# Kernel tuning notes

Measured on AMD Instinct MI355X. Metric: run time of the kernel, lower is better.

## Reference

```python
import jax, jax.numpy as jnp
import numpy as np

DIM = 192
D_STATE = 16
D_CONV = 4
EXPAND = 2
DI = EXPAND * DIM          # d_inner = 384
DT_RANK = -(-DIM // 16)    # ceil(dim/16) = 12
BSZ, T, H, W = 2, 16, 32, 32
EPS = 1e-5


def setup_inputs() -> dict:
    key = jax.random.key(0)
    ks = jax.random.split(key, 10)
    r = lambda k, s, sc=0.02: jax.random.normal(k, s, dtype=jnp.float32) * sc
    return {
        "x": jax.random.normal(ks[0], (BSZ, T, H, W, DIM), dtype=jnp.float32),
        "conv1_w": r(ks[1], (DIM, DIM, 3, 3, 3)),
        "conv1_b": jnp.zeros((DIM,), jnp.float32),
        "conv2_w": r(ks[2], (DIM, DIM, 3, 3, 3)),
        "conv2_b": jnp.zeros((DIM,), jnp.float32),
        "ln_g": jnp.ones((DIM,), jnp.float32),
        "ln_b": jnp.zeros((DIM,), jnp.float32),
        "in_proj_w": r(ks[3], (2 * DI, DIM)),
        "conv1d_w": r(ks[4], (DI, 1, D_CONV), 0.1),
        "conv1d_b": jnp.zeros((DI,), jnp.float32),
        "x_proj_w": r(ks[5], (DT_RANK + 2 * D_STATE, DI)),
        "dt_proj_w": r(ks[6], (DI, DT_RANK), 0.1),
        "dt_proj_b": r(ks[7], (DI,), 0.1),
        "A_log": jnp.log(jnp.tile(jnp.arange(1, D_STATE + 1, dtype=jnp.float32), (DI, 1))),
        "Dp": jnp.ones((DI,), jnp.float32),
        "out_proj_w": r(ks[8], (DIM, DI)),
    }


def _conv3d(x, w, b):
    y = jax.lax.conv_general_dilated(
        x, w, window_strides=(1, 1, 1), padding=((1, 1), (1, 1), (1, 1)),
        dimension_numbers=("NCDHW", "OIDHW", "NCDHW"))
    return y + b[None, :, None, None, None]


def _inorm(x):  # InstanceNorm3d, affine=False: normalize per (B,C) over spatial
    mu = jnp.mean(x, axis=(2, 3, 4), keepdims=True)
    var = jnp.var(x, axis=(2, 3, 4), keepdims=True)
    return (x - mu) * jax.lax.rsqrt(var + EPS)


def _mamba(x_norm, in_proj_w, conv1d_w, conv1d_b, x_proj_w, dt_proj_w,
           dt_proj_b, A_log, Dp, out_proj_w):
    B, L, _ = x_norm.shape
    xz = x_norm @ in_proj_w.T                      # (B, L, 2*DI)
    u, z = xz[..., :DI], xz[..., DI:]
    # causal depthwise conv1d over sequence (left pad d_conv-1)
    uc = jax.lax.conv_general_dilated(
        u.transpose(0, 2, 1), conv1d_w, window_strides=(1,),
        padding=((D_CONV - 1, 0),), dimension_numbers=("NCH", "OIH", "NCH"),
        feature_group_count=DI) + conv1d_b[None, :, None]
    u = jax.nn.silu(uc.transpose(0, 2, 1))         # (B, L, DI)
    xdb = u @ x_proj_w.T                           # (B, L, dt_rank+2*d_state)
    dt = xdb[..., :DT_RANK]
    Bm = xdb[..., DT_RANK:DT_RANK + D_STATE]       # (B, L, d_state)
    Cm = xdb[..., DT_RANK + D_STATE:]
    delta = jax.nn.softplus(dt @ dt_proj_w.T + dt_proj_b)  # (B, L, DI)
    A = -jnp.exp(A_log)                            # (DI, d_state)

    def step(h, inp):
        dlt, bt, ct, ut = inp                      # (B,DI) (B,S) (B,S) (B,DI)
        h = jnp.exp(dlt[:, :, None] * A) * h + (dlt * ut)[:, :, None] * bt[:, None, :]
        return h, jnp.einsum("bds,bs->bd", h, ct)

    h0 = jnp.zeros((B, DI, D_STATE), x_norm.dtype)
    xs = (delta.transpose(1, 0, 2), Bm.transpose(1, 0, 2),
          Cm.transpose(1, 0, 2), u.transpose(1, 0, 2))
    _, ys = jax.lax.scan(step, h0, xs)             # (L, B, DI)
    y = ys.transpose(1, 0, 2) + u * Dp
    y = y * jax.nn.silu(z)
    return y @ out_proj_w.T                        # (B, L, DIM)


def reference(x, conv1_w, conv1_b, conv2_w, conv2_b, ln_g, ln_b, in_proj_w,
              conv1d_w, conv1d_b, x_proj_w, dt_proj_w, dt_proj_b, A_log, Dp,
              out_proj_w):
    B = x.shape[0]
    xc = x.transpose(0, 4, 1, 2, 3)                # (B, C, T, H, W)
    res = xc
    x1 = jax.nn.leaky_relu(_inorm(_conv3d(xc, conv1_w, conv1_b)), 0.01)
    xc = _inorm(_conv3d(x1, conv2_w, conv2_b)) + res
    xl = xc.transpose(0, 2, 3, 4, 1)               # (B, T, H, W, C)
    # faithful to original: raw row-major reshape (B,T,H,W,C)->(B,C,THW)
    x_flat = xl.reshape(B, DIM, T * H * W).transpose(0, 2, 1)
    # LayerNorm over last dim
    mu = jnp.mean(x_flat, axis=-1, keepdims=True)
    var = jnp.var(x_flat, axis=-1, keepdims=True)
    x_norm = (x_flat - mu) * jax.lax.rsqrt(var + EPS) * ln_g + ln_b
    y = _mamba(x_norm, in_proj_w, conv1d_w, conv1d_b, x_proj_w, dt_proj_w,
               dt_proj_b, A_log, Dp, out_proj_w)
    return y.reshape(B, T, H, W, DIM)
```

## Files before the change

kernel.cpp:

```cpp
#include <hip/hip_runtime.h>


typedef unsigned short u16;
typedef __attribute__((ext_vector_type(8))) short bf16x8;
typedef __attribute__((ext_vector_type(4))) float f4;

#define MTOT 32768

__device__ __forceinline__ float b2f(u16 v){ return __uint_as_float(((unsigned)v)<<16); }
__device__ __forceinline__ u16 f2b(float f){
  unsigned u = __float_as_uint(f);
  return (u16)((u + 0x7fffu + ((u>>16)&1u)) >> 16);
}
__device__ __forceinline__ float blo(unsigned v){ return __uint_as_float(v<<16); }
__device__ __forceinline__ float bhi(unsigned v){ return __uint_as_float(v & 0xffff0000u); }
__device__ __forceinline__ unsigned pack2(float a, float b){
  return (unsigned)f2b(a) | ((unsigned)f2b(b)<<16);
}

__device__ __forceinline__ void gl16(const u16* g, u16* l){
  __builtin_amdgcn_global_load_lds((const __attribute__((address_space(1))) void*)g,
                                   (__attribute__((address_space(3))) void*)l, 16, 0, 0);
}

__global__ __launch_bounds__(256) void k_init(int* cnt, float* zp, float* stats){
  int i = blockIdx.x*256 + threadIdx.x;
  if (i == 0)   *cnt = 0;
  if (i < 128)  zp[i] = 0.f;
  if (i < 3072) stats[i] = 0.f;
}

__global__ void k_diag(float* o, float v){
  o[0] = v; o[1] = v;
  ((u16*)o)[4] = f2b(v); ((u16*)o)[5] = f2b(v);
}

__global__ __launch_bounds__(256) void k_probe(const u16* __restrict__ x, int* cnt){
  int t = threadIdx.x;
  int c = 0;
  #pragma unroll
  for (int i=0;i<16;i++){
    u16 v = x[t*16 + i];
    if (((v>>7)&0xFF) >= 0x90) c++;
  }
  if (c) atomicAdd(cnt, c);
}

__global__ __launch_bounds__(256) void k_cvt(const void* __restrict__ src, u16* __restrict__ dst,
                                             int n, const int* __restrict__ cnt){
  const int gid = blockIdx.x*256 + threadIdx.x;
  if (gid*8 >= n) return;
  if (*cnt > 64){
    const float4* s = (const float4*)src;
    float4 a = s[gid*2], b = s[gid*2+1];
    *(uint4*)(dst + gid*8) = make_uint4(pack2(a.x,a.y), pack2(a.z,a.w),
                                        pack2(b.x,b.y), pack2(b.z,b.w));
  } else {
    ((uint4*)dst)[gid] = ((const uint4*)src)[gid];
  }
}

struct SmallCvt { const void* src[13]; int n[13]; int off[13]; };

__global__ __launch_bounds__(256) void k_cvt_small(SmallCvt sc, u16* __restrict__ wc,
                                                   const int* __restrict__ cnt){
  const int t = blockIdx.y;
  const int gid = blockIdx.x*256 + threadIdx.x;
  const int n = sc.n[t];
  if (gid*8 >= n) return;
  u16* dst = wc + sc.off[t];
  if (*cnt > 64){
    const float4* s = (const float4*)sc.src[t];
    float4 a = s[gid*2], b = s[gid*2+1];
    *(uint4*)(dst + gid*8) = make_uint4(pack2(a.x,a.y), pack2(a.z,a.w),
                                        pack2(b.x,b.y), pack2(b.z,b.w));
  } else {
    *(uint4*)(dst + gid*8) = ((const uint4*)sc.src[t])[gid];
  }
}

__global__ __launch_bounds__(256) void k_wt(const void* __restrict__ w1, const void* __restrict__ w2,
                                            u16* __restrict__ b1, u16* __restrict__ b2,
                                            const int* __restrict__ cnt){
  int gid = blockIdx.x*256 + threadIdx.x;
  if (gid >= 2*995328) return;
  const bool f32 = *cnt > 64;
  int sel = gid >= 995328 ? 1 : 0;
  int lo  = gid - sel*995328;
  int co = lo / 5184, rr = lo % 5184;
  int p  = rr / 192,  ci = rr % 192;
  const void* s = sel ? w2 : w1;
  const int si = (co*192 + ci)*27 + p;
  u16 v = f32 ? f2b(((const float*)s)[si]) : ((const u16*)s)[si];
  (sel ? b2 : b1)[lo] = v;
}

__global__ __launch_bounds__(256) void k_conv(const u16* __restrict__ X, const u16* __restrict__ Bw,
                                              const u16* __restrict__ bias, u16* __restrict__ outc,
                                              float* __restrict__ sumG, float* __restrict__ sqG){
  __shared__ u16 Al[1280*8];
  __shared__ u16 Bl[1792*8];
  const int tid = threadIdx.x;
  const int m0 = blockIdx.x*128, n0 = blockIdx.y*64;
  const int bb = blockIdx.x >> 7;
  const int rem0 = m0 & 16383;
  const int t0 = rem0 >> 10, h0 = (rem0 >> 5) & 31;
  const int lane = tid&63, wv = tid>>6, wm = wv>>1, wn = wv&1, lr = lane&15, q = lane>>4;

  int aoff[5];
  #pragma unroll
  for (int j=0;j<5;j++){
    const int c = j*256 + tid;
    const int rw = c/9, cc = c%9;
    aoff[j] = (c < 1170 && cc < 8) ? (rw*192 + cc*8) : 0;
  }
  int boff[7];
  #pragma unroll
  for (int j=0;j<7;j++){
    const int c = j*256 + tid;
    const int rw = c/9, cc = c%9;
    boff[j] = (c < 1728 && cc < 8) ? ((n0 + (rw & 63))*5184 + (rw >> 6)*192 + cc*8) : 0;
  }

  const f4 z4 = {0.f,0.f,0.f,0.f};
  const bf16x8 z8 = {0,0,0,0,0,0,0,0};
  f4 acc[4][2];
  #pragma unroll
  for (int i=0;i<4;i++){
    #pragma unroll
    for (int j=0;j<2;j++) acc[i][j] = z4;
  }

  for (int s=0; s<27; ++s){
    const int dtdh = s/3, sub = s - dtdh*3;
    const int dt = dtdh/3 - 1, dh = dtdh%3 - 1;
    __syncthreads();
    const u16* Ab = X + (ptrdiff_t)(m0 - 1 + dt*1024 + dh*32)*192 + sub*64;
    #pragma unroll
    for (int j=0;j<5;j++) gl16(Ab + aoff[j], Al + (size_t)(j*256 + tid)*8);
    const u16* Bb = Bw + dtdh*576 + sub*64;
    #pragma unroll
    for (int j=0;j<7;j++) gl16(Bb + boff[j], Bl + (size_t)(j*256 + tid)*8);
    __syncthreads();
    const bool tval = ((unsigned)(t0 + dt) < 16u);
    const bool hv0 = ((unsigned)(h0 + wm*2     + dh) < 32u);
    const bool hv1 = ((unsigned)(h0 + wm*2 + 1 + dh) < 32u);
    if (tval){
      #pragma unroll
      for (int kt=0; kt<2; ++kt){
        bf16x8 bv[3][2];
        #pragma unroll
        for (int tp=0;tp<3;tp++){
          #pragma unroll
          for (int j=0;j<2;j++)
            bv[tp][j] = *(const bf16x8*)&Bl[(tp*64 + wn*32 + j*16 + lr)*72 + kt*32 + q*8];
        }
        #pragma unroll
        for (int i=0;i<4;i++){
          const bool hok = (i<2) ? hv0 : hv1;
          if (!hok) continue;
          const int crow = wm*64 + i*16 + lr;
          #pragma unroll
          for (int tp=0;tp<3;tp++){
            bf16x8 av = *(const bf16x8*)&Al[(crow + tp)*72 + kt*32 + q*8];
            if (tp==0 && (i&1)==0) av = (lr==0)  ? z8 : av;
            if (tp==2 && (i&1)==1) av = (lr==15) ? z8 : av;
            acc[i][0] = __builtin_amdgcn_mfma_f32_16x16x32_bf16(av, bv[tp][0], acc[i][0], 0,0,0);
            acc[i][1] = __builtin_amdgcn_mfma_f32_16x16x32_bf16(av, bv[tp][1], acc[i][1], 0,0,0);
          }
        }
      }
    }
  }

  float psum[2] = {0.f,0.f}, psq[2] = {0.f,0.f};
  #pragma unroll
  for (int j=0;j<2;j++){
    const int col = n0 + wn*32 + j*16 + lr;
    const float bvl = b2f(bias[col]);
    #pragma unroll
    for (int i=0;i<4;i++){
      const int row0 = m0 + wm*64 + i*16 + q*4;
      #pragma unroll
      for (int g=0; g<4; ++g){
        const float v = acc[i][j][g] + bvl;
        outc[(size_t)(row0+g)*192 + col] = f2b(v);
        psum[j] += v; psq[j] += v*v;
      }
    }
  }
  __syncthreads();
  float* red = (float*)Al;
  if (tid < 128) red[tid] = 0.f;
  __syncthreads();
  #pragma unroll
  for (int j=0;j<2;j++){
    const int cl = wn*32 + j*16 + lr;
    atomicAdd(&red[cl], psum[j]);
    atomicAdd(&red[64+cl], psq[j]);
  }
  __syncthreads();
  if (tid < 64){
    atomicAdd(&sumG[bb*192 + n0 + tid], red[tid]);
    atomicAdd(&sqG[bb*192 + n0 + tid], red[64+tid]);
  }
}

template<int EPI>
__global__ __launch_bounds__(256) void k_gemm(const u16* __restrict__ A, const u16* __restrict__ Bm,
                                              const int K, const int NB,
                                              void* __restrict__ o0, void* __restrict__ o1,
                                              const u16* __restrict__ zp,
                                              const int* __restrict__ cnt){
  __shared__ u16 Al[128*104];
  __shared__ u16 Bl[64*104];
  const int tid = threadIdx.x;
  const int m0 = blockIdx.x*128, n0 = blockIdx.y*64;
  const int r = tid>>1, half = tid&1;
  const u16* arow = A + ((size_t)(m0+r)*K + half*48);
  const int bn = tid>>2, bk = tid&3;
  const bool bval = (n0+bn) < NB;
  const u16* brow = Bm + ((size_t)(n0+bn)*K + bk*24);
  const int lane = tid&63, wv = tid>>6, wm = wv>>1, wn = wv&1, lr = lane&15, q = lane>>4;
  const f4 z4 = {0.f,0.f,0.f,0.f};
  f4 acc[4][2];
  #pragma unroll
  for (int i=0;i<4;i++){
    #pragma unroll
    for (int j=0;j<2;j++) acc[i][j] = z4;
  }
  for (int k0=0; k0<K; k0+=96){
    const u16* as = arow + k0;
    const u16* bs = bval ? (brow + k0) : zp;
    __syncthreads();
    #pragma unroll
    for (int i=0;i<6;i++)
      *(uint4*)&Al[r*104 + half*48 + i*8] = *(const uint4*)(as + i*8);
    #pragma unroll
    for (int i=0;i<3;i++)
      *(uint4*)&Bl[bn*104 + bk*24 + i*8] = *(const uint4*)(bs + i*8);
    __syncthreads();
    #pragma unroll
    for (int kt=0; kt<3; ++kt){
      bf16x8 av[4], bv[2];
      #pragma unroll
      for (int i=0;i<4;i++) av[i] = *(const bf16x8*)&Al[(wm*64 + i*16 + lr)*104 + kt*32 + q*8];
      #pragma unroll
      for (int j=0;j<2;j++) bv[j] = *(const bf16x8*)&Bl[(wn*32 + j*16 + lr)*104 + kt*32 + q*8];
      #pragma unroll
      for (int i=0;i<4;i++){
        #pragma unroll
        for (int j=0;j<2;j++)
          acc[i][j] = __builtin_amdgcn_mfma_f32_16x16x32_bf16(av[i], bv[j], acc[i][j], 0,0,0);
      }
    }
  }
  const bool f32o = (EPI == 2) && (*cnt > 64);
  #pragma unroll
  for (int j=0;j<2;j++){
    const int col = n0 + wn*32 + j*16 + lr;
    #pragma unroll
    for (int i=0;i<4;i++){
      const int row0 = m0 + wm*64 + i*16 + q*4;
      #pragma unroll
      for (int g=0; g<4; ++g){
        const int row = row0 + g;
        const float v = acc[i][j][g];
        if (EPI == 0){
          if (col < 384) ((u16*)o0)[(size_t)row*384 + col] = f2b(v);
          else           ((u16*)o1)[(size_t)row*384 + (col-384)] = f2b(v);
        } else if (EPI == 1){
          if (col < 44)  ((float*)o0)[(size_t)row*44 + col] = v;
        } else {
          if (f32o) ((float*)o0)[(size_t)row*192 + col] = v;
          else      ((u16*) o0)[(size_t)row*192 + col] = f2b(v);
        }
      }
    }
  }
}

__global__ __launch_bounds__(384) void k_infin(const float* __restrict__ s, const float* __restrict__ s2,
                                               float* __restrict__ mr){
  const int i = threadIdx.x;
  const float mean = s[i]*(1.f/16384.f);
  const float var  = s2[i]*(1.f/16384.f) - mean*mean;
  mr[i]     = mean;
  mr[384+i] = rsqrtf(var + 1e-5f);
}

__global__ __launch_bounds__(256) void k_inapply(const u16* __restrict__ craw, const float* __restrict__ mr,
                                                 const u16* __restrict__ resid, u16* __restrict__ outp,
                                                 const int mode){
  const int gid = blockIdx.x*256 + threadIdx.x;
  const size_t base = (size_t)gid*8;
  const int mrow = gid/24;
  const int c0 = (gid%24)*8;
  const int b = mrow >> 14;
  const uint4 rv = *(const uint4*)(craw + base);
  float vv[8] = {blo(rv.x),bhi(rv.x),blo(rv.y),bhi(rv.y),blo(rv.z),bhi(rv.z),blo(rv.w),bhi(rv.w)};
  uint4 xv;
  float rr[8];
  if (mode == 2){
    xv = *(const uint4*)(resid + base);
    rr[0]=blo(xv.x); rr[1]=bhi(xv.x); rr[2]=blo(xv.y); rr[3]=bhi(xv.y);
    rr[4]=blo(xv.z); rr[5]=bhi(xv.z); rr[6]=blo(xv.w); rr[7]=bhi(xv.w);
  }
  unsigned pk[4];
  #pragma unroll
  for (int k2=0;k2<4;k2++){
    const int c = c0 + 2*k2;
    float a0 = (vv[2*k2]   - mr[b*192+c])  * mr[384 + b*192 + c];
    float a1 = (vv[2*k2+1] - mr[b*192+c+1])* mr[384 + b*192 + c+1];
    if (mode == 1){ a0 = a0 > 0.f ? a0 : 0.01f*a0; a1 = a1 > 0.f ? a1 : 0.01f*a1; }
    else          { a0 += rr[2*k2]; a1 += rr[2*k2+1]; }
    pk[k2] = pack2(a0, a1);
  }
  *(uint4*)(outp + base) = make_uint4(pk[0],pk[1],pk[2],pk[3]);
}

__global__ __launch_bounds__(128) void k_ln(const u16* __restrict__ F, const u16* __restrict__ g,
                                            const u16* __restrict__ bb, u16* __restrict__ xn){
  __shared__ u16 S[192*128];
  const int tid = threadIdx.x;
  const int b = blockIdx.y;
  const int l0 = blockIdx.x*128;
  const u16* Fb = F + (size_t)b*3145728;
  for (int qi = tid; qi < 3072; qi += 128){
    int c = qi >> 4, o = (qi & 15)*8;
    *(uint4*)&S[c*128 + o] = *(const uint4*)(Fb + (size_t)c*16384 + l0 + o);
  }
  __syncthreads();
  float sum = 0.f, sq = 0.f;
  for (int c=0;c<192;c++){ float v = b2f(S[c*128 + tid]); sum += v; sq += v*v; }
  const float mean = sum*(1.f/192.f);
  const float rs = rsqrtf(sq*(1.f/192.f) - mean*mean + 1e-5f);
  u16* dst = xn + ((size_t)(b*16384 + l0 + tid))*192;
  for (int c0=0;c0<192;c0+=8){
    unsigned pk[4];
    #pragma unroll
    for (int k2=0;k2<4;k2++){
      int c = c0 + 2*k2;
      float v0 = (b2f(S[(c  )*128+tid]) - mean)*rs*b2f(g[c  ]) + b2f(bb[c  ]);
      float v1 = (b2f(S[(c+1)*128+tid]) - mean)*rs*b2f(g[c+1]) + b2f(bb[c+1]);
      pk[k2] = pack2(v0, v1);
    }
    *(uint4*)(dst + c0) = make_uint4(pk[0],pk[1],pk[2],pk[3]);
  }
}

__global__ __launch_bounds__(256) void k_conv1d(const u16* __restrict__ u, const u16* __restrict__ w,
                                                const u16* __restrict__ bias, u16* __restrict__ up){
  const int gid = blockIdx.x*256 + threadIdx.x;
  const int mrow = gid/48, d8 = (gid%48)*8;
  const int l = mrow & 16383;
  float acc[8];
  #pragma unroll
  for (int k=0;k<8;k++) acc[k] = b2f(bias[d8+k]);
  float wk[4][8];
  #pragma unroll
  for (int dd=0;dd<8;dd++){
    uint2 tw = *(const uint2*)(w + (size_t)(d8+dd)*4);
    wk[0][dd]=blo(tw.x); wk[1][dd]=bhi(tw.x); wk[2][dd]=blo(tw.y); wk[3][dd]=bhi(tw.y);
  }
  #pragma unroll
  for (int k=0;k<4;k++){
    if (l - 3 + k < 0) continue;
    uint4 tv = *(const uint4*)(u + ((size_t)(mrow-3+k))*384 + d8);
    float uv[8] = {blo(tv.x),bhi(tv.x),blo(tv.y),bhi(tv.y),blo(tv.z),bhi(tv.z),blo(tv.w),bhi(tv.w)};
    #pragma unroll
    for (int dd=0;dd<8;dd++) acc[dd] += uv[dd]*wk[k][dd];
  }
  unsigned pk[4];
  #pragma unroll
  for (int k2=0;k2<4;k2++){
    float a0 = acc[2*k2], a1 = acc[2*k2+1];
    a0 = a0/(1.f + __expf(-a0));
    a1 = a1/(1.f + __expf(-a1));
    pk[k2] = pack2(a0, a1);
  }
  *(uint4*)(up + (size_t)mrow*384 + d8) = make_uint4(pk[0],pk[1],pk[2],pk[3]);
}

__global__ __launch_bounds__(192) void k_scan1(const float* __restrict__ xdb, const u16* __restrict__ up,
                                               const u16* __restrict__ dtw, const u16* __restrict__ dtb,
                                               const u16* __restrict__ alog,
                                               float* __restrict__ P, float* __restrict__ Q){
  __shared__ float xdbS[64*44];
  const int tid = threadIdx.x;
  const int chunk = blockIdx.x, b = blockIdx.y;
  const int d = blockIdx.z*192 + tid;
  const size_t mbase = (size_t)b*16384 + chunk*64;
  const float* xs = xdb + mbase*44;
  for (int qi=tid; qi<704; qi+=192)
    *(float4*)&xdbS[qi*4] = *(const float4*)(xs + (size_t)qi*4);
  float w[12];
  #pragma unroll
  for (int i=0;i<12;i++) w[i] = b2f(dtw[d*12+i]);
  const float dtbv = b2f(dtb[d]);
  float Av[16];
  #pragma unroll
  for (int s=0;s<16;s++) Av[s] = -__expf(b2f(alog[d*16+s]));
  float pp[16], qq[16];
  #pragma unroll
  for (int s=0;s<16;s++){ pp[s]=1.f; qq[s]=0.f; }
  const u16* uptr = up + mbase*384 + d;
  __syncthreads();
  for (int l=0;l<64;l++){
    const float* row = &xdbS[l*44];
    const float4 r0 = *(const float4*)(row);
    const float4 r1 = *(const float4*)(row+4);
    const float4 r2 = *(const float4*)(row+8);
    float a = dtbv + r0.x*w[0]+r0.y*w[1]+r0.z*w[2]+r0.w*w[3]
                   + r1.x*w[4]+r1.y*w[5]+r1.z*w[6]+r1.w*w[7]
                   + r2.x*w[8]+r2.y*w[9]+r2.z*w[10]+r2.w*w[11];
    const float dl = a > 20.f ? a : __logf(1.f + __expf(a));
    const float uv = b2f(uptr[(size_t)l*384]);
    const float dlu = dl*uv;
    const float4 B0 = *(const float4*)(row+12);
    const float4 B1 = *(const float4*)(row+16);
    const float4 B2 = *(const float4*)(row+20);
    const float4 B3 = *(const float4*)(row+24);
    const float Bv[16] = {B0.x,B0.y,B0.z,B0.w,B1.x,B1.y,B1.z,B1.w,
                          B2.x,B2.y,B2.z,B2.w,B3.x,B3.y,B3.z,B3.w};
    #pragma unroll
    for (int s=0;s<16;s++){
      const float as = __expf(dl*Av[s]);
      pp[s] *= as;
      qq[s] = as*qq[s] + dlu*Bv[s];
    }
  }
  const size_t o = (((size_t)b*256 + chunk)*384 + d)*16;
  float* Po = P + o; float* Qo = Q + o;
  *(float4*)(Po+ 0) = make_float4(pp[0],pp[1],pp[2],pp[3]);
  *(float4*)(Po+ 4) = make_float4(pp[4],pp[5],pp[6],pp[7]);
  *(float4*)(Po+ 8) = make_float4(pp[8],pp[9],pp[10],pp[11]);
  *(float4*)(Po+12) = make_float4(pp[12],pp[13],pp[14],pp[15]);
  *(float4*)(Qo+ 0) = make_float4(qq[0],qq[1],qq[2],qq[3]);
  *(float4*)(Qo+ 4) = make_float4(qq[4],qq[5],qq[6],qq[7]);
  *(float4*)(Qo+ 8) = make_float4(qq[8],qq[9],qq[10],qq[11]);
  *(float4*)(Qo+12) = make_float4(qq[12],qq[13],qq[14],qq[15]);
}

__global__ __launch_bounds__(256) void k_scan2(const float* __restrict__ P, const float* __restrict__ Q,
                                               float* __restrict__ hin){
  const int gid = blockIdx.x*256 + threadIdx.x;
  const int b = gid / 6144, ds = gid % 6144;
  const size_t base = (size_t)b*1572864 + ds;
  float h = 0.f;
  for (int g2=0; g2<256; ++g2){
    const size_t idx = base + (size_t)g2*6144;
    hin[idx] = h;
    h = P[idx]*h + Q[idx];
  }
}

__global__ __launch_bounds__(192) void k_scan3(const float* __restrict__ xdb, const u16* __restrict__ up,
                                               const u16* __restrict__ zb,
                                               const u16* __restrict__ dtw, const u16* __restrict__ dtb,
                                               const u16* __restrict__ alog, const u16* __restrict__ dp,
                                               const float* __restrict__ hin, u16* __restrict__ yg){
  __shared__ float xdbS[64*44];
  const int tid = threadIdx.x;
  const int chunk = blockIdx.x, b = blockIdx.y;
  const int d = blockIdx.z*192 + tid;
  const size_t mbase = (size_t)b*16384 + chunk*64;
  const float* xs = xdb + mbase*44;
  for (int qi=tid; qi<704; qi+=192)
    *(float4*)&xdbS[qi*4] = *(const float4*)(xs + (size_t)qi*4);
  float w[12];
  #pragma unroll
  for (int i=0;i<12;i++) w[i] = b2f(dtw[d*12+i]);
  const float dtbv = b2f(dtb[d]);
  float Av[16];
  #pragma unroll
  for (int s=0;s<16;s++) Av[s] = -__expf(b2f(alog[d*16+s]));
  const float Dv = b2f(dp[d]);
  float h[16];
  {
    const float* hi = hin + (((size_t)b*256 + chunk)*384 + d)*16;
    const float4 h0 = *(const float4*)(hi+0);
    const float4 h1 = *(const float4*)(hi+4);
    const float4 h2 = *(const float4*)(hi+8);
    const float4 h3 = *(const float4*)(hi+12);
    h[0]=h0.x;h[1]=h0.y;h[2]=h0.z;h[3]=h0.w;
    h[4]=h1.x;h[5]=h1.y;h[6]=h1.z;h[7]=h1.w;
    h[8]=h2.x;h[9]=h2.y;h[10]=h2.z;h[11]=h2.w;
    h[12]=h3.x;h[13]=h3.y;h[14]=h3.z;h[15]=h3.w;
  }
  const u16* uptr = up + mbase*384 + d;
  const u16* zptr = zb + mbase*384 + d;
  u16* yptr = yg + mbase*384 + d;
  __syncthreads();
  for (int l=0;l<64;l++){
    const float* row = &xdbS[l*44];
    const float4 r0 = *(const float4*)(row);
    const float4 r1 = *(const float4*)(row+4);
    const float4 r2 = *(const float4*)(row+8);
    float a = dtbv + r0.x*w[0]+r0.y*w[1]+r0.z*w[2]+r0.w*w[3]
                   + r1.x*w[4]+r1.y*w[5]+r1.z*w[6]+r1.w*w[7]
                   + r2.x*w[8]+r2.y*w[9]+r2.z*w[10]+r2.w*w[11];
    const float dl = a > 20.f ? a : __logf(1.f + __expf(a));
    const float uv = b2f(uptr[(size_t)l*384]);
    const float dlu = dl*uv;
    const float4 B0 = *(const float4*)(row+12);
    const float4 B1 = *(const float4*)(row+16);
    const float4 B2 = *(const float4*)(row+20);
    const float4 B3 = *(const float4*)(row+24);
    const float4 C0 = *(const float4*)(row+28);
    const float4 C1 = *(const float4*)(row+32);
    const float4 C2 = *(const float4*)(row+36);
    const float4 C3 = *(const float4*)(row+40);
    const float Bv[16] = {B0.x,B0.y,B0.z,B0.w,B1.x,B1.y,B1.z,B1.w,
                          B2.x,B2.y,B2.z,B2.w,B3.x,B3.y,B3.z,B3.w};
    const float Cv[16] = {C0.x,C0.y,C0.z,C0.w,C1.x,C1.y,C1.z,C1.w,
                          C2.x,C2.y,C2.z,C2.w,C3.x,C3.y,C3.z,C3.w};
    float ct = 0.f;
    #pragma unroll
    for (int s=0;s<16;s++){
      const float as = __expf(dl*Av[s]);
      h[s] = as*h[s] + dlu*Bv[s];
      ct += h[s]*Cv[s];
    }
    const float yv = ct + uv*Dv;
    const float zv = b2f(zptr[(size_t)l*384]);
    yptr[(size_t)l*384] = f2b(yv * (zv/(1.f + __expf(-zv))));
  }
}

extern "C" void kernel_launch(void* const* d_in, const int* in_sizes, int n_in,
                              void* d_out, int out_size, void* d_ws, size_t ws_size,
                              hipStream_t stream){
  (void)in_sizes; (void)n_in; (void)out_size;
  const u16* x = (const u16*)d_in[0];
  u16* outp = (u16*)d_out;

  char* ws = (char*)d_ws;
  size_t off = 0;
  auto alloc = [&](size_t bytes)->void*{
    void* p = (void*)(ws + off);
    off += (bytes + 255) & ~(size_t)255;
    return p;
  };
  int*   cnt   = (int*)  alloc(256);
  u16*   zp    = (u16*)  alloc(512);
  float* stats = (float*)alloc((size_t)3072*4);
  u16*   wc    = (u16*)  alloc((size_t)252288*2);
  u16*   Bw1   = (u16*)  alloc((size_t)995328*2);
  u16*   Bw2   = (u16*)  alloc((size_t)995328*2);
  u16*   xc    = (u16*)  alloc((size_t)MTOT*192*2);
  u16*   craw  = (u16*)  alloc((size_t)MTOT*192*2);
  u16*   bx    = (u16*)  alloc((size_t)MTOT*192*2);
  u16*   ubuf  = (u16*)  alloc((size_t)MTOT*384*2);
  u16*   zbuf  = (u16*)  alloc((size_t)MTOT*384*2);
  u16*   upost = (u16*)  alloc((size_t)MTOT*384*2);
  const size_t NEEDED = off;

  if (ws_size < NEEDED){
    k_diag<<<1,1,0,stream>>>((float*)d_out, (float)(ws_size >> 20));
    return;
  }

  u16* xnorm = craw;
  float* xdb = (float*)xc;
  float* P   = (float*)ubuf;
  float* Q   = (float*)(ubuf + 6291456);
  float* hin = (float*)bx;
  u16*   yg  = upost;

  float* sum1 = stats;        float* sq1 = stats+384;  float* mr1 = stats+768;
  float* sum2 = stats+1536;   float* sq2 = stats+1920; float* mr2 = stats+2304;

  SmallCvt sc;
  const int srcIdx[13] = {2,4,5,6,7,8,9,10,11,12,13,14,15};
  const int ns[13]     = {192,192,192,192,147456,1536,384,16896,4608,384,6144,384,73728};
  const int offs[13]   = {0,192,384,576,768,148224,149760,150144,167040,171648,172032,178176,178560};
  for (int i=0;i<13;i++){ sc.src[i]=d_in[srcIdx[i]]; sc.n[i]=ns[i]; sc.off[i]=offs[i]; }
  const u16 *c1b=wc+0, *c2b=wc+192, *lng=wc+384, *lnb=wc+576, *ipw=wc+768,
            *c1dw=wc+148224, *c1db=wc+149760, *xpw=wc+150144, *dtw=wc+167040,
            *dtb=wc+171648, *alog=wc+172032, *dp=wc+178176, *opw=wc+178560;

  k_init<<<12,256,0,stream>>>(cnt, (float*)zp, stats);
  k_probe<<<1,256,0,stream>>>(x, cnt);
  k_cvt<<<3072,256,0,stream>>>(d_in[0], xc, MTOT*192, cnt);
  k_cvt_small<<<dim3(72,13),256,0,stream>>>(sc, wc, cnt);
  k_wt<<<7776,256,0,stream>>>(d_in[1], d_in[3], Bw1, Bw2, cnt);

  k_conv<<<dim3(256,3),256,0,stream>>>(xc, Bw1, c1b, craw, sum1, sq1);
  k_infin<<<1,384,0,stream>>>(sum1, sq1, mr1);
  k_inapply<<<3072,256,0,stream>>>(craw, mr1, xc, bx, 1);
  k_conv<<<dim3(256,3),256,0,stream>>>(bx, Bw2, c2b, craw, sum2, sq2);
  k_infin<<<1,384,0,stream>>>(sum2, sq2, mr2);
  k_inapply<<<3072,256,0,stream>>>(craw, mr2, xc, bx, 2);

  k_ln<<<dim3(128,2),128,0,stream>>>(bx, lng, lnb, xnorm);
  k_gemm<0><<<dim3(256,12),256,0,stream>>>(xnorm, ipw, 192, 768, ubuf, zbuf, zp, cnt);
  k_conv1d<<<6144,256,0,stream>>>(ubuf, c1dw, c1db, upost);
  k_gemm<1><<<dim3(256,1),256,0,stream>>>(upost, xpw, 384, 44, xdb, nullptr, zp, cnt);
  k_scan1<<<dim3(256,2,2),192,0,stream>>>(xdb, upost, dtw, dtb, alog, P, Q);
  k_scan2<<<48,256,0,stream>>>(P, Q, hin);
  k_scan3<<<dim3(256,2,2),192,0,stream>>>(xdb, upost, zbuf, dtw, dtb, alog, dp, hin, yg);
  k_gemm<2><<<dim3(256,3),256,0,stream>>>(yg, opw, 384, 192, outp, nullptr, zp, cnt);
}
```

Before: 555.1 us.

## Split scan state across thread pairs, batch scan2 loads, skip out-of-range conv taps

The selective-scan kernels now give each channel to two threads, each holding 8 of the 16 states. This doubles the grid and cuts per-thread register pressure, with the C-dot partials combined by a shuffle. k_scan2 loads eight P/Q values before running the serial recurrence, so memory latency overlaps the dependent chain. The 3D conv skips loading and syncing for temporal taps that fall outside the volume, instead of loading the tile and then ignoring it. The cost is duplicated dt/softplus work per thread pair and half-idle lanes on the output store.

Result: no change. 555.5 us (+0.1%).

```diff
diff --git a/kernel.cpp b/kernel.cpp
--- a/kernel.cpp
+++ b/kernel.cpp
@@ -134,6 +134,8 @@
   for (int s=0; s<27; ++s){
     const int dtdh = s/3, sub = s - dtdh*3;
     const int dt = dtdh/3 - 1, dh = dtdh%3 - 1;
+    const bool tval = ((unsigned)(t0 + dt) < 16u);
+    if (!tval) continue;
     __syncthreads();
     const u16* Ab = X + (ptrdiff_t)(m0 - 1 + dt*1024 + dh*32)*192 + sub*64;
     #pragma unroll
@@ -142,32 +144,29 @@
     #pragma unroll
     for (int j=0;j<7;j++) gl16(Bb + boff[j], Bl + (size_t)(j*256 + tid)*8);
     __syncthreads();
-    const bool tval = ((unsigned)(t0 + dt) < 16u);
     const bool hv0 = ((unsigned)(h0 + wm*2     + dh) < 32u);
     const bool hv1 = ((unsigned)(h0 + wm*2 + 1 + dh) < 32u);
-    if (tval){
+    #pragma unroll
+    for (int kt=0; kt<2; ++kt){
+      bf16x8 bv[3][2];
       #pragma unroll
-      for (int kt=0; kt<2; ++kt){
-        bf16x8 bv[3][2];
+      for (int tp=0;tp<3;tp++){
+        #pragma unroll
+        for (int j=0;j<2;j++)
+          bv[tp][j] = *(const bf16x8*)&Bl[(tp*64 + wn*32 + j*16 + lr)*72 + kt*32 + q*8];
+      }
+      #pragma unroll
+      for (int i=0;i<4;i++){
+        const bool hok = (i<2) ? hv0 : hv1;
+        if (!hok) continue;
+        const int crow = wm*64 + i*16 + lr;
         #pragma unroll
         for (int tp=0;tp<3;tp++){
-          #pragma unroll
-          for (int j=0;j<2;j++)
-            bv[tp][j] = *(const bf16x8*)&Bl[(tp*64 + wn*32 + j*16 + lr)*72 + kt*32 + q*8];
-        }
-        #pragma unroll
-        for (int i=0;i<4;i++){
-          const bool hok = (i<2) ? hv0 : hv1;
-          if (!hok) continue;
-          const int crow = wm*64 + i*16 + lr;
-          #pragma unroll
-          for (int tp=0;tp<3;tp++){
-            bf16x8 av = *(const bf16x8*)&Al[(crow + tp)*72 + kt*32 + q*8];
-            if (tp==0 && (i&1)==0) av = (lr==0)  ? z8 : av;
-            if (tp==2 && (i&1)==1) av = (lr==15) ? z8 : av;
-            acc[i][0] = __builtin_amdgcn_mfma_f32_16x16x32_bf16(av, bv[tp][0], acc[i][0], 0,0,0);
-            acc[i][1] = __builtin_amdgcn_mfma_f32_16x16x32_bf16(av, bv[tp][1], acc[i][1], 0,0,0);
-          }
+          bf16x8 av = *(const bf16x8*)&Al[(crow + tp)*72 + kt*32 + q*8];
+          if (tp==0 && (i&1)==0) av = (lr==0)  ? z8 : av;
+          if (tp==2 && (i&1)==1) av = (lr==15) ? z8 : av;
+          acc[i][0] = __builtin_amdgcn_mfma_f32_16x16x32_bf16(av, bv[tp][0], acc[i][0], 0,0,0);
+          acc[i][1] = __builtin_amdgcn_mfma_f32_16x16x32_bf16(av, bv[tp][1], acc[i][1], 0,0,0);
         }
       }
     }
@@ -389,7 +388,8 @@
   __shared__ float xdbS[64*44];
   const int tid = threadIdx.x;
   const int chunk = blockIdx.x, b = blockIdx.y;
-  const int d = blockIdx.z*192 + tid;
+  const int d = blockIdx.z*96 + (tid>>1);
+  const int s0 = (tid & 1)*8;
   const size_t mbase = (size_t)b*16384 + chunk*64;
   const float* xs = xdb + mbase*44;
   for (int qi=tid; qi<704; qi+=192)
@@ -398,12 +398,12 @@
   #pragma unroll
   for (int i=0;i<12;i++) w[i] = b2f(dtw[d*12+i]);
   const float dtbv = b2f(dtb[d]);
-  float Av[16];
-  #pragma unroll
-  for (int s=0;s<16;s++) Av[s] = -__expf(b2f(alog[d*16+s]));
-  float pp[16], qq[16];
-  #pragma unroll
-  for (int s=0;s<16;s++){ pp[s]=1.f; qq[s]=0.f; }
+  float Av[8];
+  #pragma unroll
+  for (int s=0;s<8;s++) Av[s] = -__expf(b2f(alog[d*16 + s0 + s]));
+  float pp[8], qq[8];
+  #pragma unroll
+  for (int s=0;s<8;s++){ pp[s]=1.f; qq[s]=0.f; }
   const u16* uptr = up + mbase*384 + d;
   __syncthreads();
   for (int l=0;l<64;l++){
@@ -417,29 +417,22 @@
     const float dl = a > 20.f ? a : __logf(1.f + __expf(a));
     const float uv = b2f(uptr[(size_t)l*384]);
     const float dlu = dl*uv;
-    const float4 B0 = *(const float4*)(row+12);
-    const float4 B1 = *(const float4*)(row+16);
-    const float4 B2 = *(const float4*)(row+20);
-    const float4 B3 = *(const float4*)(row+24);
-    const float Bv[16] = {B0.x,B0.y,B0.z,B0.w,B1.x,B1.y,B1.z,B1.w,
-                          B2.x,B2.y,B2.z,B2.w,B3.x,B3.y,B3.z,B3.w};
-    #pragma unroll
-    for (int s=0;s<16;s++){
+    const float4 B0 = *(const float4*)(row+12+s0);
+    const float4 B1 = *(const float4*)(row+16+s0);
+    const float Bv[8] = {B0.x,B0.y,B0.z,B0.w,B1.x,B1.y,B1.z,B1.w};
+    #pragma unroll
+    for (int s=0;s<8;s++){
       const float as = __expf(dl*Av[s]);
       pp[s] *= as;
       qq[s] = as*qq[s] + dlu*Bv[s];
     }
   }
-  const size_t o = (((size_t)b*256 + chunk)*384 + d)*16;
+  const size_t o = (((size_t)b*256 + chunk)*384 + d)*16 + s0;
   float* Po = P + o; float* Qo = Q + o;
-  *(float4*)(Po+ 0) = make_float4(pp[0],pp[1],pp[2],pp[3]);
-  *(float4*)(Po+ 4) = make_float4(pp[4],pp[5],pp[6],pp[7]);
-  *(float4*)(Po+ 8) = make_float4(pp[8],pp[9],pp[10],pp[11]);
-  *(float4*)(Po+12) = make_float4(pp[12],pp[13],pp[14],pp[15]);
-  *(float4*)(Qo+ 0) = make_float4(qq[0],qq[1],qq[2],qq[3]);
-  *(float4*)(Qo+ 4) = make_float4(qq[4],qq[5],qq[6],qq[7]);
-  *(float4*)(Qo+ 8) = make_float4(qq[8],qq[9],qq[10],qq[11]);
-  *(float4*)(Qo+12) = make_float4(qq[12],qq[13],qq[14],qq[15]);
+  *(float4*)(Po+0) = make_float4(pp[0],pp[1],pp[2],pp[3]);
+  *(float4*)(Po+4) = make_float4(pp[4],pp[5],pp[6],pp[7]);
+  *(float4*)(Qo+0) = make_float4(qq[0],qq[1],qq[2],qq[3]);
+  *(float4*)(Qo+4) = make_float4(qq[4],qq[5],qq[6],qq[7]);
 }
 
 __global__ __launch_bounds__(256) void k_scan2(const float* __restrict__ P, const float* __restrict__ Q,
@@ -448,10 +441,19 @@
   const int b = gid / 6144, ds = gid % 6144;
   const size_t base = (size_t)b*1572864 + ds;
   float h = 0.f;
-  for (int g2=0; g2<256; ++g2){
-    const size_t idx = base + (size_t)g2*6144;
-    hin[idx] = h;
-    h = P[idx]*h + Q[idx];
+  for (int g=0; g<32; ++g){
+    float p8[8], q8[8];
+    #pragma unroll
+    for (int k=0;k<8;k++){
+      const size_t idx = base + (size_t)(g*8+k)*6144;
+      p8[k] = P[idx]; q8[k] = Q[idx];
+    }
+    #pragma unroll
+    for (int k=0;k<8;k++){
+      const size_t idx = base + (size_t)(g*8+k)*6144;
+      hin[idx] = h;
+      h = p8[k]*h + q8[k];
+    }
   }
 }
 
@@ -463,7 +465,9 @@
   __shared__ float xdbS[64*44];
   const int tid = threadIdx.x;
   const int chunk = blockIdx.x, b = blockIdx.y;
-  const int d = blockIdx.z*192 + tid;
+  const int d = blockIdx.z*96 + (tid>>1);
+  const int shalf = tid & 1;
+  const int s0 = shalf*8;
   const size_t mbase = (size_t)b*16384 + chunk*64;
   const float* xs = xdb + mbase*44;
   for (int qi=tid; qi<704; qi+=192)
@@ -472,21 +476,17 @@
   #pragma unroll
   for (int i=0;i<12;i++) w[i] = b2f(dtw[d*12+i]);
   const float dtbv = b2f(dtb[d]);
-  float Av[16];
-  #pragma unroll
-  for (int s=0;s<16;s++) Av[s] = -__expf(b2f(alog[d*16+s]));
+  float Av[8];
+  #pragma unroll
+  for (int s=0;s<8;s++) Av[s] = -__expf(b2f(alog[d*16 + s0 + s]));
   const float Dv = b2f(dp[d]);
-  float h[16];
+  float h[8];
   {
-    const float* hi = hin + (((size_t)b*256 + chunk)*384 + d)*16;
+    const float* hi = hin + (((size_t)b*256 + chunk)*384 + d)*16 + s0;
     const float4 h0 = *(const float4*)(hi+0);
     const float4 h1 = *(const float4*)(hi+4);
-    const float4 h2 = *(const float4*)(hi+8);
-    const float4 h3 = *(const float4*)(hi+12);
     h[0]=h0.x;h[1]=h0.y;h[2]=h0.z;h[3]=h0.w;
     h[4]=h1.x;h[5]=h1.y;h[6]=h1.z;h[7]=h1.w;
-    h[8]=h2.x;h[9]=h2.y;h[10]=h2.z;h[11]=h2.w;
-    h[12]=h3.x;h[13]=h3.y;h[14]=h3.z;h[15]=h3.w;
   }
   const u16* uptr = up + mbase*384 + d;
   const u16* zptr = zb + mbase*384 + d;
@@ -503,28 +503,25 @@
     const float dl = a > 20.f ? a : __logf(1.f + __expf(a));
     const float uv = b2f(uptr[(size_t)l*384]);
     const float dlu = dl*uv;
-    const float4 B0 = *(const float4*)(row+12);
-    const float4 B1 = *(const float4*)(row+16);
-    const float4 B2 = *(const float4*)(row+20);
-    const float4 B3 = *(const float4*)(row+24);
-    const float4 C0 = *(const float4*)(row+28);
-    const float4 C1 = *(const float4*)(row+32);
-    const float4 C2 = *(const float4*)(row+36);
-    const float4 C3 = *(const float4*)(row+40);
-    const float Bv[16] = {B0.x,B0.y,B0.z,B0.w,B1.x,B1.y,B1.z,B1.w,
-                          B2.x,B2.y,B2.z,B2.w,B3.x,B3.y,B3.z,B3.w};
-    const float Cv[16] = {C0.x,C0.y,C0.z,C0.w,C1.x,C1.y,C1.z,C1.w,
-                          C2.x,C2.y,C2.z,C2.w,C3.x,C3.y,C3.z,C3.w};
+    const float4 B0 = *(const float4*)(row+12+s0);
+    const float4 B1 = *(const float4*)(row+16+s0);
+    const float4 C0 = *(const float4*)(row+28+s0);
+    const float4 C1 = *(const float4*)(row+32+s0);
+    const float Bv[8] = {B0.x,B0.y,B0.z,B0.w,B1.x,B1.y,B1.z,B1.w};
+    const float Cv[8] = {C0.x,C0.y,C0.z,C0.w,C1.x,C1.y,C1.z,C1.w};
     float ct = 0.f;
     #pragma unroll
-    for (int s=0;s<16;s++){
+    for (int s=0;s<8;s++){
       const float as = __expf(dl*Av[s]);
       h[s] = as*h[s] + dlu*Bv[s];
       ct += h[s]*Cv[s];
     }
-    const float yv = ct + uv*Dv;
-    const float zv = b2f(zptr[(size_t)l*384]);
-    yptr[(size_t)l*384] = f2b(yv * (zv/(1.f + __expf(-zv))));
+    ct += __shfl_xor(ct, 1);
+    if (shalf == 0){
+      const float yv = ct + uv*Dv;
+      const float zv = b2f(zptr[(size_t)l*384]);
+      yptr[(size_t)l*384] = f2b(yv * (zv/(1.f + __expf(-zv))));
+    }
   }
 }
 
@@ -597,8 +594,8 @@
   k_gemm<0><<<dim3(256,12),256,0,stream>>>(xnorm, ipw, 192, 768, ubuf, zbuf, zp, cnt);
   k_conv1d<<<6144,256,0,stream>>>(ubuf, c1dw, c1db, upost);
   k_gemm<1><<<dim3(256,1),256,0,stream>>>(upost, xpw, 384, 44, xdb, nullptr, zp, cnt);
-  k_scan1<<<dim3(256,2,2),192,0,stream>>>(xdb, upost, dtw, dtb, alog, P, Q);
+  k_scan1<<<dim3(256,2,4),192,0,stream>>>(xdb, upost, dtw, dtb, alog, P, Q);
   k_scan2<<<48,256,0,stream>>>(P, Q, hin);
-  k_scan3<<<dim3(256,2,2),192,0,stream>>>(xdb, upost, zbuf, dtw, dtb, alog, dp, hin, yg);
+  k_scan3<<<dim3(256,2,4),192,0,stream>>>(xdb, upost, zbuf, dtw, dtb, alog, dp, hin, yg);
   k_gemm<2><<<dim3(256,3),256,0,stream>>>(yg, opw, 384, 192, outp, nullptr, zp, cnt);
 }
```
